# Kernel optimization log

Measured on AMD Instinct MI355X. Metric: run time of the kernel, lower is better.

The kernel has to match this reference:

```python
import jax, jax.numpy as jnp
import numpy as np

N, E, F_IN, H, C = 10000, 640000, 128, 128, 40


def setup_inputs() -> dict:
    key = jax.random.key(0)
    ks = jax.random.split(key, 8)
    x = jax.random.normal(ks[0], (N, F_IN), dtype=jnp.float32)
    edge_index = jax.random.randint(ks[1], (2, E), 0, N, dtype=jnp.int64)
    W1 = jax.random.normal(ks[2], (F_IN, H), dtype=jnp.float32) / np.sqrt(F_IN)
    b1 = jnp.zeros((H,), dtype=jnp.float32)
    W2 = jax.random.normal(ks[3], (H, H), dtype=jnp.float32) / np.sqrt(H)
    b2 = jnp.zeros((H,), dtype=jnp.float32)
    Wc = jax.random.normal(ks[4], (H, C), dtype=jnp.float32) / np.sqrt(H)
    bc = jnp.zeros((C,), dtype=jnp.float32)
    return {"x": x, "edge_index": edge_index, "W1": W1, "b1": b1,
            "W2": W2, "b2": b2, "Wc": Wc, "bc": bc}


def _gcn_conv(x, src, dst, norm, W, b):
    # GCNConv: out = D^{-1/2}(A+I)D^{-1/2} (x @ W) + b
    h = x @ W                               # [N, H]
    msg = h[src] * norm[:, None]            # gather + per-edge normalize
    out = jax.ops.segment_sum(msg, dst, num_segments=N)  # scatter-add
    return out + b


def reference(x, edge_index, W1, b1, W2, b2, Wc, bc):
    # add self-loops (as PyG GCNConv does by default)
    loops = jnp.arange(N, dtype=edge_index.dtype)
    src = jnp.concatenate([edge_index[0], loops])   # [E+N]
    dst = jnp.concatenate([edge_index[1], loops])   # [E+N]
    # symmetric normalization deg^{-1/2} with self-loops included
    deg = jax.ops.segment_sum(jnp.ones_like(dst, dtype=x.dtype), dst, num_segments=N)
    dinv = jax.lax.rsqrt(deg)                       # deg >= 1 due to self-loops
    norm = dinv[src] * dinv[dst]                    # [E+N]

    h = _gcn_conv(x, src, dst, norm, W1, b1)
    h = jax.nn.relu(h)
    h = _gcn_conv(h, src, dst, norm, W2, b2)
    logits = h @ Wc + bc                            # [N, C]
    return jax.nn.log_softmax(logits, axis=1)
```

## Files before the change

### kernel.cpp

```cpp
#include <hip/hip_runtime.h>
#include <hip/hip_fp16.h>
#include <math.h>

#define FDIM 128
#define CDIM 40
#define DMAX 192
#define NMAX 10240
#define SLICE_SHIFT 14
#define SLICE_SZ (1 << SLICE_SHIFT)

__device__ __forceinline__ uint2 pack_half4(float4 v) {
    __half2 p0 = __float22half2_rn(make_float2(v.x, v.y));
    __half2 p1 = __float22half2_rn(make_float2(v.z, v.w));
    uint2 u;
    u.x = *(unsigned int*)&p0;
    u.y = *(unsigned int*)&p1;
    return u;
}

__device__ __forceinline__ void unpack_add4(float acc[8], uint4 r) {
    __half2* p = (__half2*)&r;
    #pragma unroll
    for (int q = 0; q < 4; ++q) {
        float2 f = __half22float2(p[q]);
        acc[2 * q]     += f.x;
        acc[2 * q + 1] += f.y;
    }
}

__global__ __launch_bounds__(256) void k_hist(
        const int* __restrict__ dst, unsigned short* __restrict__ lrank,
        int* __restrict__ cnt, int e, int n) {
    __shared__ int h[NMAX];
    int tid = threadIdx.x;
    for (int i = tid; i < n; i += 256) h[i] = 0;
    __syncthreads();
    int base = (int)blockIdx.x << SLICE_SHIFT;
    int end = base + SLICE_SZ; if (end > e) end = e;
    for (int i = base + tid * 4; i < end; i += 1024) {
        if (i + 3 < end) {
            int4 d = *(const int4*)(dst + i);
            int p0 = atomicAdd(&h[d.x], 1);
            int p1 = atomicAdd(&h[d.y], 1);
            int p2 = atomicAdd(&h[d.z], 1);
            int p3 = atomicAdd(&h[d.w], 1);
            ushort4 r;
            r.x = (unsigned short)p0; r.y = (unsigned short)p1;
            r.z = (unsigned short)p2; r.w = (unsigned short)p3;
            *(ushort4*)(lrank + i) = r;
        } else {
            for (int k = i; k < end; ++k)
                lrank[k] = (unsigned short)atomicAdd(&h[dst[k]], 1);
        }
    }
    __syncthreads();
    int* c = cnt + (size_t)blockIdx.x * n;
    for (int i = tid; i < n; i += 256) c[i] = h[i];
}

__global__ __launch_bounds__(256) void k_scan(
        int* __restrict__ cnt, int* __restrict__ deg, int nslice, int n) {
    int v = blockIdx.x * 256 + threadIdx.x;
    if (v >= n) return;
    int s = 0;
    for (int b = 0; b < nslice; ++b) {
        int t = cnt[(size_t)b * n + v];
        cnt[(size_t)b * n + v] = s;
        s += t;
    }
    deg[v] = s;
}

__global__ __launch_bounds__(256) void k_mega(
        const float* __restrict__ A, const float* __restrict__ W,
        const int* __restrict__ deg, uint2* __restrict__ h16, int n,
        const int* __restrict__ src, const int* __restrict__ dst,
        const unsigned short* __restrict__ lrank, const int* __restrict__ base,
        unsigned short* __restrict__ col, int e, int gemm_blocks) {
    __shared__ float As[32][FDIM];
    int tid = threadIdx.x;
    if ((int)blockIdx.x < gemm_blocks) {
        int r0 = blockIdx.x * 32;
        for (int t = tid; t < 32 * 32; t += 256) {
            int r = t >> 5, c4 = t & 31;
            int gr = r0 + r;
            float4 v = make_float4(0.f, 0.f, 0.f, 0.f);
            if (gr < n) v = ((const float4*)A)[(size_t)gr * 32 + c4];
            ((float4*)As[r])[c4] = v;
        }
        __syncthreads();
        int cb = (tid & 31) * 4;
        int rb = (tid >> 5) * 4;
        float4 acc0 = make_float4(0,0,0,0), acc1 = acc0, acc2 = acc0, acc3 = acc0;
        for (int k = 0; k < FDIM; ++k) {
            float4 w = *(const float4*)(W + k * FDIM + cb);
            float a0 = As[rb + 0][k], a1 = As[rb + 1][k];
            float a2 = As[rb + 2][k], a3 = As[rb + 3][k];
            acc0.x += a0 * w.x; acc0.y += a0 * w.y; acc0.z += a0 * w.z; acc0.w += a0 * w.w;
            acc1.x += a1 * w.x; acc1.y += a1 * w.y; acc1.z += a1 * w.z; acc1.w += a1 * w.w;
            acc2.x += a2 * w.x; acc2.y += a2 * w.y; acc2.z += a2 * w.z; acc2.w += a2 * w.w;
            acc3.x += a3 * w.x; acc3.y += a3 * w.y; acc3.z += a3 * w.z; acc3.w += a3 * w.w;
        }
        float4 accs[4] = {acc0, acc1, acc2, acc3};
        #pragma unroll
        for (int i = 0; i < 4; ++i) {
            int gr = r0 + rb + i;
            if (gr < n) {
                float dinv = rsqrtf((float)(deg[gr] + 1));
                float4 v = accs[i];
                v.x *= dinv; v.y *= dinv; v.z *= dinv; v.w *= dinv;
                h16[(size_t)gr * 32 + (cb >> 2)] = pack_half4(v);
            }
        }
    } else {
        int g = ((int)blockIdx.x - gemm_blocks) * 256 + tid;
        int i4 = g * 4;
        if (i4 + 3 < e) {
            const int* bs = base + (size_t)(i4 >> SLICE_SHIFT) * n;
            int4 d = ((const int4*)dst)[g];
            int4 s = ((const int4*)src)[g];
            ushort4 lr = ((const ushort4*)lrank)[g];
            int p0 = bs[d.x] + lr.x;
            int p1 = bs[d.y] + lr.y;
            int p2 = bs[d.z] + lr.z;
            int p3 = bs[d.w] + lr.w;
            if (p0 < DMAX) col[(size_t)d.x * DMAX + p0] = (unsigned short)s.x;
            if (p1 < DMAX) col[(size_t)d.y * DMAX + p1] = (unsigned short)s.y;
            if (p2 < DMAX) col[(size_t)d.z * DMAX + p2] = (unsigned short)s.z;
            if (p3 < DMAX) col[(size_t)d.w * DMAX + p3] = (unsigned short)s.w;
        } else if (i4 < e) {
            for (int k = i4; k < e; ++k) {
                int d = dst[k];
                int p = base[(size_t)(k >> SLICE_SHIFT) * n + d] + lrank[k];
                if (p < DMAX) col[(size_t)d * DMAX + p] = (unsigned short)src[k];
            }
        }
    }
}

template <bool RELU>
__device__ __forceinline__ void agg_gather(
        float out8[8], const uint4* __restrict__ hs,
        const unsigned short* __restrict__ col, const int* __restrict__ deg,
        const float* __restrict__ bias, int node, int l) {
    int dn = deg[node];
    float dinv = rsqrtf((float)(dn + 1));
    if (dn > DMAX) dn = DMAX;
    const uint4* cl8 = (const uint4*)(col + (size_t)node * DMAX);
    float a0[8], a1[8];
    #pragma unroll
    for (int q = 0; q < 8; ++q) { a0[q] = 0.f; a1[q] = 0.f; }
    unpack_add4(a0, hs[(size_t)node * 16 + l]);
    int j = 0;
    for (; j + 16 <= dn; j += 16) {
        uint4 cA = cl8[(j >> 3) + 0];
        uint4 cB = cl8[(j >> 3) + 1];
        int s0 = cA.x & 0xFFFF, s1 = cA.x >> 16;
        int s2 = cA.y & 0xFFFF, s3 = cA.y >> 16;
        int s4 = cA.z & 0xFFFF, s5 = cA.z >> 16;
        int s6 = cA.w & 0xFFFF, s7 = cA.w >> 16;
        int s8 = cB.x & 0xFFFF, s9 = cB.x >> 16;
        int sa = cB.y & 0xFFFF, sb = cB.y >> 16;
        int sc = cB.z & 0xFFFF, sd = cB.z >> 16;
        int se = cB.w & 0xFFFF, sf = cB.w >> 16;
        uint4 q0 = hs[(size_t)s0 * 16 + l];
        uint4 q1 = hs[(size_t)s1 * 16 + l];
        uint4 q2 = hs[(size_t)s2 * 16 + l];
        uint4 q3 = hs[(size_t)s3 * 16 + l];
        uint4 q4 = hs[(size_t)s4 * 16 + l];
        uint4 q5 = hs[(size_t)s5 * 16 + l];
        uint4 q6 = hs[(size_t)s6 * 16 + l];
        uint4 q7 = hs[(size_t)s7 * 16 + l];
        uint4 q8 = hs[(size_t)s8 * 16 + l];
        uint4 q9 = hs[(size_t)s9 * 16 + l];
        uint4 qa = hs[(size_t)sa * 16 + l];
        uint4 qb = hs[(size_t)sb * 16 + l];
        uint4 qc = hs[(size_t)sc * 16 + l];
        uint4 qd = hs[(size_t)sd * 16 + l];
        uint4 qe = hs[(size_t)se * 16 + l];
        uint4 qf = hs[(size_t)sf * 16 + l];
        unpack_add4(a0, q0); unpack_add4(a1, q1);
        unpack_add4(a0, q2); unpack_add4(a1, q3);
        unpack_add4(a0, q4); unpack_add4(a1, q5);
        unpack_add4(a0, q6); unpack_add4(a1, q7);
        unpack_add4(a0, q8); unpack_add4(a1, q9);
        unpack_add4(a0, qa); unpack_add4(a1, qb);
        unpack_add4(a0, qc); unpack_add4(a1, qd);
        unpack_add4(a0, qe); unpack_add4(a1, qf);
    }
    for (; j + 8 <= dn; j += 8) {
        uint4 c = cl8[j >> 3];
        int s0 = c.x & 0xFFFF, s1 = c.x >> 16;
        int s2 = c.y & 0xFFFF, s3 = c.y >> 16;
        int s4 = c.z & 0xFFFF, s5 = c.z >> 16;
        int s6 = c.w & 0xFFFF, s7 = c.w >> 16;
        uint4 q0 = hs[(size_t)s0 * 16 + l];
        uint4 q1 = hs[(size_t)s1 * 16 + l];
        uint4 q2 = hs[(size_t)s2 * 16 + l];
        uint4 q3 = hs[(size_t)s3 * 16 + l];
        uint4 q4 = hs[(size_t)s4 * 16 + l];
        uint4 q5 = hs[(size_t)s5 * 16 + l];
        uint4 q6 = hs[(size_t)s6 * 16 + l];
        uint4 q7 = hs[(size_t)s7 * 16 + l];
        unpack_add4(a0, q0); unpack_add4(a1, q1);
        unpack_add4(a0, q2); unpack_add4(a1, q3);
        unpack_add4(a0, q4); unpack_add4(a1, q5);
        unpack_add4(a0, q6); unpack_add4(a1, q7);
    }
    const unsigned short* cl = col + (size_t)node * DMAX;
    for (; j < dn; ++j) unpack_add4(a0, hs[(size_t)cl[j] * 16 + l]);
    float4 b0 = ((const float4*)bias)[2 * l];
    float4 b1 = ((const float4*)bias)[2 * l + 1];
    float bb[8] = {b0.x, b0.y, b0.z, b0.w, b1.x, b1.y, b1.z, b1.w};
    #pragma unroll
    for (int q = 0; q < 8; ++q) {
        float v = dinv * (a0[q] + a1[q]) + bb[q];
        out8[q] = RELU ? fmaxf(v, 0.f) : v;
    }
}

__global__ __launch_bounds__(128) void k_agg_gemm(
        const uint4* __restrict__ hs1, const unsigned short* __restrict__ col,
        const int* __restrict__ deg, const float* __restrict__ b1,
        const float* __restrict__ W2, uint2* __restrict__ hs2, int n) {
    __shared__ float As[8][FDIM + 4];
    __shared__ float dl[8];
    int tid = threadIdx.x;
    int grp = tid >> 4, l = tid & 15;
    int node = blockIdx.x * 8 + grp;
    if (node < n) {
        float r8[8];
        agg_gather<true>(r8, hs1, col, deg, b1, node, l);
        float4* dst4 = (float4*)&As[grp][8 * l];
        dst4[0] = make_float4(r8[0], r8[1], r8[2], r8[3]);
        dst4[1] = make_float4(r8[4], r8[5], r8[6], r8[7]);
        if (l == 0) dl[grp] = rsqrtf((float)(deg[node] + 1));
    }
    __syncthreads();
    int cb = (tid & 31) * 4;
    int rb = (tid >> 5) * 2;
    float4 acc0 = make_float4(0,0,0,0), acc1 = acc0;
    for (int k = 0; k < FDIM; ++k) {
        float4 w = *(const float4*)(W2 + k * FDIM + cb);
        float x0 = As[rb][k], x1 = As[rb + 1][k];
        acc0.x += x0 * w.x; acc0.y += x0 * w.y; acc0.z += x0 * w.z; acc0.w += x0 * w.w;
        acc1.x += x1 * w.x; acc1.y += x1 * w.y; acc1.z += x1 * w.z; acc1.w += x1 * w.w;
    }
    int g0 = blockIdx.x * 8 + rb;
    if (g0 < n) {
        float s = dl[rb];
        float4 v = acc0;
        v.x *= s; v.y *= s; v.z *= s; v.w *= s;
        hs2[(size_t)g0 * 32 + (cb >> 2)] = pack_half4(v);
    }
    if (g0 + 1 < n) {
        float s = dl[rb + 1];
        float4 v = acc1;
        v.x *= s; v.y *= s; v.z *= s; v.w *= s;
        hs2[(size_t)(g0 + 1) * 32 + (cb >> 2)] = pack_half4(v);
    }
}

__global__ __launch_bounds__(128) void k_agg_cls(
        const uint4* __restrict__ hs2, const unsigned short* __restrict__ col,
        const int* __restrict__ deg, const float* __restrict__ b2,
        const float* __restrict__ Wc, const float* __restrict__ bc,
        float* __restrict__ out, int n) {
    __shared__ float As[8][FDIM + 4];
    int tid = threadIdx.x;
    int grp = tid >> 4, l = tid & 15;
    int node = blockIdx.x * 8 + grp;
    if (node < n) {
        float r8[8];
        agg_gather<false>(r8, hs2, col, deg, b2, node, l);
        float4* dst4 = (float4*)&As[grp][8 * l];
        dst4[0] = make_float4(r8[0], r8[1], r8[2], r8[3]);
        dst4[1] = make_float4(r8[4], r8[5], r8[6], r8[7]);
    }
    __syncthreads();
    int wv = tid >> 6, lane = tid & 63;
    #pragma unroll
    for (int ii = 0; ii < 4; ++ii) {
        int li = wv * 4 + ii;
        int nd = blockIdx.x * 8 + li;
        if (nd >= n) continue;
        const float* row = As[li];
        int c = (lane < CDIM) ? lane : (lane - 24);
        float acc = bc[c];
        for (int k = 0; k < FDIM; k += 4) {
            float a0 = row[k + 0], a1 = row[k + 1];
            float a2 = row[k + 2], a3 = row[k + 3];
            acc += a0 * Wc[(k + 0) * CDIM + c];
            acc += a1 * Wc[(k + 1) * CDIM + c];
            acc += a2 * Wc[(k + 2) * CDIM + c];
            acc += a3 * Wc[(k + 3) * CDIM + c];
        }
        float lv = (lane < CDIM) ? acc : -INFINITY;
        float m = lv;
        for (int off = 32; off > 0; off >>= 1) m = fmaxf(m, __shfl_down(m, off));
        m = __shfl(m, 0);
        float e = (lane < CDIM) ? expf(lv - m) : 0.0f;
        float s = e;
        for (int off = 32; off > 0; off >>= 1) s += __shfl_down(s, off);
        s = __shfl(s, 0);
        if (lane < CDIM) out[(size_t)nd * CDIM + lane] = lv - m - logf(s);
    }
}


extern "C" void kernel_launch(void* const* d_in, const int* in_sizes, int n_in,
                              void* d_out, int out_size, void* d_ws, size_t ws_size,
                              hipStream_t stream) {
    const float* x  = (const float*)d_in[0];
    const int*   ei = (const int*)d_in[1];
    const float* W1 = (const float*)d_in[2];
    const float* b1 = (const float*)d_in[3];
    const float* W2 = (const float*)d_in[4];
    const float* b2 = (const float*)d_in[5];
    const float* Wc = (const float*)d_in[6];
    const float* bc = (const float*)d_in[7];
    float* out = (float*)d_out;

    const int N = in_sizes[0] / FDIM;
    const int E = in_sizes[1] / 2;
    const int* srcp = ei;
    const int* dstp = ei + E;
    const int NSLICE = (E + SLICE_SZ - 1) >> SLICE_SHIFT;

    char* ws = (char*)d_ws;
    auto alloc = [&](size_t bytes) {
        char* p = ws;
        ws += (bytes + 255) & ~(size_t)255;
        return p;
    };
    int*            deg   = (int*)           alloc((size_t)N * 4);
    int*            cnt   = (int*)           alloc((size_t)NSLICE * N * 4);
    unsigned short* lrank = (unsigned short*)alloc((size_t)E * 2);
    unsigned short* col   = (unsigned short*)alloc((size_t)N * DMAX * 2);
    uint4*          h1h   = (uint4*)         alloc((size_t)N * 256);
    uint4*          h2h   = (uint4*)         alloc((size_t)N * 256);

    k_hist<<<NSLICE, 256, 0, stream>>>(dstp, lrank, cnt, E, N);

    k_scan<<<(N + 255) / 256, 256, 0, stream>>>(cnt, deg, NSLICE, N);

    int gb = (N + 31) / 32;
    int fb = (E / 4 + 255) / 256;
    k_mega<<<gb + fb, 256, 0, stream>>>(
        x, W1, deg, (uint2*)h1h, N, srcp, dstp, lrank, cnt, col, E, gb);

    k_agg_gemm<<<(N + 7) / 8, 128, 0, stream>>>(
        h1h, col, deg, b1, W2, (uint2*)h2h, N);

    k_agg_cls<<<(N + 7) / 8, 128, 0, stream>>>(
        h2h, col, deg, b2, Wc, bc, out, N);
}
```

Baseline: 159.5 us.

## Overlap layer-1 GEMM with histogram, shrink slices, use fma_mix accumulation

Moves the first x@W1 GEMM into the histogram kernel as extra blocks that write fp32 results, so it no longer waits on the degree scan. The later fill kernel gains blocks that scale by dinv and pack the result to fp16. Slices shrink from 16K to 4K edges to give the histogram more parallel blocks. The aggregation loop now prefetches column indices one step ahead and accumulates fp16 with inline v_fma_mix_f32 instead of converting then adding. The costs are an extra fp32 N×128 round trip through memory and a scan over four times as many slices.

```diff
diff --git a/kernel.cpp b/kernel.cpp
--- a/kernel.cpp
+++ b/kernel.cpp
@@ -6,7 +6,7 @@
 #define CDIM 40
 #define DMAX 192
 #define NMAX 10240
-#define SLICE_SHIFT 14
+#define SLICE_SHIFT 12
 #define SLICE_SZ (1 << SLICE_SHIFT)
 
 __device__ __forceinline__ uint2 pack_half4(float4 v) {
@@ -18,69 +18,54 @@
     return u;
 }
 
-__device__ __forceinline__ void unpack_add4(float acc[8], uint4 r) {
-    __half2* p = (__half2*)&r;
-    #pragma unroll
-    for (int q = 0; q < 4; ++q) {
-        float2 f = __half22float2(p[q]);
-        acc[2 * q]     += f.x;
-        acc[2 * q + 1] += f.y;
-    }
+__device__ __forceinline__ void fmix_add4(float a[8], uint4 r) {
+    asm("v_fma_mix_f32 %0, %8, 1.0, %0 op_sel:[0,0,0] op_sel_hi:[1,0,0]\n\t"
+        "v_fma_mix_f32 %1, %8, 1.0, %1 op_sel:[1,0,0] op_sel_hi:[1,0,0]\n\t"
+        "v_fma_mix_f32 %2, %9, 1.0, %2 op_sel:[0,0,0] op_sel_hi:[1,0,0]\n\t"
+        "v_fma_mix_f32 %3, %9, 1.0, %3 op_sel:[1,0,0] op_sel_hi:[1,0,0]\n\t"
+        "v_fma_mix_f32 %4, %10, 1.0, %4 op_sel:[0,0,0] op_sel_hi:[1,0,0]\n\t"
+        "v_fma_mix_f32 %5, %10, 1.0, %5 op_sel:[1,0,0] op_sel_hi:[1,0,0]\n\t"
+        "v_fma_mix_f32 %6, %11, 1.0, %6 op_sel:[0,0,0] op_sel_hi:[1,0,0]\n\t"
+        "v_fma_mix_f32 %7, %11, 1.0, %7 op_sel:[1,0,0] op_sel_hi:[1,0,0]"
+        : "+v"(a[0]), "+v"(a[1]), "+v"(a[2]), "+v"(a[3]),
+          "+v"(a[4]), "+v"(a[5]), "+v"(a[6]), "+v"(a[7])
+        : "v"(r.x), "v"(r.y), "v"(r.z), "v"(r.w));
 }
 
 __global__ __launch_bounds__(256) void k_hist(
         const int* __restrict__ dst, unsigned short* __restrict__ lrank,
-        int* __restrict__ cnt, int e, int n) {
+        int* __restrict__ cnt, int e, int n, int nslice,
+        const float* __restrict__ A, const float* __restrict__ W,
+        float* __restrict__ h1f) {
     __shared__ int h[NMAX];
     int tid = threadIdx.x;
-    for (int i = tid; i < n; i += 256) h[i] = 0;
-    __syncthreads();
-    int base = (int)blockIdx.x << SLICE_SHIFT;
-    int end = base + SLICE_SZ; if (end > e) end = e;
-    for (int i = base + tid * 4; i < end; i += 1024) {
-        if (i + 3 < end) {
-            int4 d = *(const int4*)(dst + i);
-            int p0 = atomicAdd(&h[d.x], 1);
-            int p1 = atomicAdd(&h[d.y], 1);
-            int p2 = atomicAdd(&h[d.z], 1);
-            int p3 = atomicAdd(&h[d.w], 1);
-            ushort4 r;
-            r.x = (unsigned short)p0; r.y = (unsigned short)p1;
-            r.z = (unsigned short)p2; r.w = (unsigned short)p3;
-            *(ushort4*)(lrank + i) = r;
-        } else {
-            for (int k = i; k < end; ++k)
-                lrank[k] = (unsigned short)atomicAdd(&h[dst[k]], 1);
-        }
-    }
-    __syncthreads();
-    int* c = cnt + (size_t)blockIdx.x * n;
-    for (int i = tid; i < n; i += 256) c[i] = h[i];
-}
-
-__global__ __launch_bounds__(256) void k_scan(
-        int* __restrict__ cnt, int* __restrict__ deg, int nslice, int n) {
-    int v = blockIdx.x * 256 + threadIdx.x;
-    if (v >= n) return;
-    int s = 0;
-    for (int b = 0; b < nslice; ++b) {
-        int t = cnt[(size_t)b * n + v];
-        cnt[(size_t)b * n + v] = s;
-        s += t;
-    }
-    deg[v] = s;
-}
-
-__global__ __launch_bounds__(256) void k_mega(
-        const float* __restrict__ A, const float* __restrict__ W,
-        const int* __restrict__ deg, uint2* __restrict__ h16, int n,
-        const int* __restrict__ src, const int* __restrict__ dst,
-        const unsigned short* __restrict__ lrank, const int* __restrict__ base,
-        unsigned short* __restrict__ col, int e, int gemm_blocks) {
-    __shared__ float As[32][FDIM];
-    int tid = threadIdx.x;
-    if ((int)blockIdx.x < gemm_blocks) {
-        int r0 = blockIdx.x * 32;
+    if ((int)blockIdx.x < nslice) {
+        for (int i = tid; i < n; i += 256) h[i] = 0;
+        __syncthreads();
+        int base = (int)blockIdx.x << SLICE_SHIFT;
+        int end = base + SLICE_SZ; if (end > e) end = e;
+        for (int i = base + tid * 4; i < end; i += 1024) {
+            if (i + 3 < end) {
+                int4 d = *(const int4*)(dst + i);
+                int p0 = atomicAdd(&h[d.x], 1);
+                int p1 = atomicAdd(&h[d.y], 1);
+                int p2 = atomicAdd(&h[d.z], 1);
+                int p3 = atomicAdd(&h[d.w], 1);
+                ushort4 r;
+                r.x = (unsigned short)p0; r.y = (unsigned short)p1;
+                r.z = (unsigned short)p2; r.w = (unsigned short)p3;
+                *(ushort4*)(lrank + i) = r;
+            } else {
+                for (int k = i; k < end; ++k)
+                    lrank[k] = (unsigned short)atomicAdd(&h[dst[k]], 1);
+            }
+        }
+        __syncthreads();
+        int* c = cnt + (size_t)blockIdx.x * n;
+        for (int i = tid; i < n; i += 256) c[i] = h[i];
+    } else {
+        float (*As)[FDIM] = (float (*)[FDIM])h;
+        int r0 = ((int)blockIdx.x - nslice) * 32;
         for (int t = tid; t < 32 * 32; t += 256) {
             int r = t >> 5, c4 = t & 31;
             int gr = r0 + r;
@@ -105,15 +90,33 @@
         #pragma unroll
         for (int i = 0; i < 4; ++i) {
             int gr = r0 + rb + i;
-            if (gr < n) {
-                float dinv = rsqrtf((float)(deg[gr] + 1));
-                float4 v = accs[i];
-                v.x *= dinv; v.y *= dinv; v.z *= dinv; v.w *= dinv;
-                h16[(size_t)gr * 32 + (cb >> 2)] = pack_half4(v);
-            }
-        }
-    } else {
-        int g = ((int)blockIdx.x - gemm_blocks) * 256 + tid;
+            if (gr < n) ((float4*)h1f)[(size_t)gr * 32 + (cb >> 2)] = accs[i];
+        }
+    }
+}
+
+__global__ __launch_bounds__(256) void k_scan(
+        int* __restrict__ cnt, int* __restrict__ deg, int nslice, int n) {
+    int v = blockIdx.x * 256 + threadIdx.x;
+    if (v >= n) return;
+    int s = 0;
+    for (int b = 0; b < nslice; ++b) {
+        int t = cnt[(size_t)b * n + v];
+        cnt[(size_t)b * n + v] = s;
+        s += t;
+    }
+    deg[v] = s;
+}
+
+__global__ __launch_bounds__(256) void k_mega(
+        const int* __restrict__ src, const int* __restrict__ dst,
+        const unsigned short* __restrict__ lrank, const int* __restrict__ base,
+        unsigned short* __restrict__ col, int e,
+        const float* __restrict__ h1f, const int* __restrict__ deg,
+        uint2* __restrict__ h16, int n, int fill_blocks) {
+    int tid = threadIdx.x;
+    if ((int)blockIdx.x < fill_blocks) {
+        int g = (int)blockIdx.x * 256 + tid;
         int i4 = g * 4;
         if (i4 + 3 < e) {
             const int* bs = base + (size_t)(i4 >> SLICE_SHIFT) * n;
@@ -130,10 +133,21 @@
             if (p3 < DMAX) col[(size_t)d.w * DMAX + p3] = (unsigned short)s.w;
         } else if (i4 < e) {
             for (int k = i4; k < e; ++k) {
-                int d = dst[k];
-                int p = base[(size_t)(k >> SLICE_SHIFT) * n + d] + lrank[k];
-                if (p < DMAX) col[(size_t)d * DMAX + p] = (unsigned short)src[k];
+                int dd = dst[k];
+                int p = base[(size_t)(k >> SLICE_SHIFT) * n + dd] + lrank[k];
+                if (p < DMAX) col[(size_t)dd * DMAX + p] = (unsigned short)src[k];
             }
+        }
+    } else {
+        int g = ((int)blockIdx.x - fill_blocks) * 256 + tid;
+        int t4 = n * 32;
+        int stride = ((int)gridDim.x - fill_blocks) * 256;
+        for (int idx = g; idx < t4; idx += stride) {
+            int node = idx >> 5;
+            float dinv = rsqrtf((float)(deg[node] + 1));
+            float4 v = ((const float4*)h1f)[idx];
+            v.x *= dinv; v.y *= dinv; v.z *= dinv; v.w *= dinv;
+            h16[idx] = pack_half4(v);
         }
     }
 }
@@ -150,43 +164,48 @@
     float a0[8], a1[8];
     #pragma unroll
     for (int q = 0; q < 8; ++q) { a0[q] = 0.f; a1[q] = 0.f; }
-    unpack_add4(a0, hs[(size_t)node * 16 + l]);
+    fmix_add4(a0, hs[(size_t)node * 16 + l]);
     int j = 0;
-    for (; j + 16 <= dn; j += 16) {
-        uint4 cA = cl8[(j >> 3) + 0];
-        uint4 cB = cl8[(j >> 3) + 1];
-        int s0 = cA.x & 0xFFFF, s1 = cA.x >> 16;
-        int s2 = cA.y & 0xFFFF, s3 = cA.y >> 16;
-        int s4 = cA.z & 0xFFFF, s5 = cA.z >> 16;
-        int s6 = cA.w & 0xFFFF, s7 = cA.w >> 16;
-        int s8 = cB.x & 0xFFFF, s9 = cB.x >> 16;
-        int sa = cB.y & 0xFFFF, sb = cB.y >> 16;
-        int sc = cB.z & 0xFFFF, sd = cB.z >> 16;
-        int se = cB.w & 0xFFFF, sf = cB.w >> 16;
-        uint4 q0 = hs[(size_t)s0 * 16 + l];
-        uint4 q1 = hs[(size_t)s1 * 16 + l];
-        uint4 q2 = hs[(size_t)s2 * 16 + l];
-        uint4 q3 = hs[(size_t)s3 * 16 + l];
-        uint4 q4 = hs[(size_t)s4 * 16 + l];
-        uint4 q5 = hs[(size_t)s5 * 16 + l];
-        uint4 q6 = hs[(size_t)s6 * 16 + l];
-        uint4 q7 = hs[(size_t)s7 * 16 + l];
-        uint4 q8 = hs[(size_t)s8 * 16 + l];
-        uint4 q9 = hs[(size_t)s9 * 16 + l];
-        uint4 qa = hs[(size_t)sa * 16 + l];
-        uint4 qb = hs[(size_t)sb * 16 + l];
-        uint4 qc = hs[(size_t)sc * 16 + l];
-        uint4 qd = hs[(size_t)sd * 16 + l];
-        uint4 qe = hs[(size_t)se * 16 + l];
-        uint4 qf = hs[(size_t)sf * 16 + l];
-        unpack_add4(a0, q0); unpack_add4(a1, q1);
-        unpack_add4(a0, q2); unpack_add4(a1, q3);
-        unpack_add4(a0, q4); unpack_add4(a1, q5);
-        unpack_add4(a0, q6); unpack_add4(a1, q7);
-        unpack_add4(a0, q8); unpack_add4(a1, q9);
-        unpack_add4(a0, qa); unpack_add4(a1, qb);
-        unpack_add4(a0, qc); unpack_add4(a1, qd);
-        unpack_add4(a0, qe); unpack_add4(a1, qf);
+    if (j + 16 <= dn) {
+        uint4 cA = cl8[0];
+        uint4 cB = cl8[1];
+        for (; j + 16 <= dn; j += 16) {
+            uint4 nA = cl8[(j >> 3) + 2];
+            uint4 nB = cl8[(j >> 3) + 3];
+            int s0 = cA.x & 0xFFFF, s1 = cA.x >> 16;
+            int s2 = cA.y & 0xFFFF, s3 = cA.y >> 16;
+            int s4 = cA.z & 0xFFFF, s5 = cA.z >> 16;
+            int s6 = cA.w & 0xFFFF, s7 = cA.w >> 16;
+            int s8 = cB.x & 0xFFFF, s9 = cB.x >> 16;
+            int sa = cB.y & 0xFFFF, sb = cB.y >> 16;
+            int sc = cB.z & 0xFFFF, sd = cB.z >> 16;
+            int se = cB.w & 0xFFFF, sf = cB.w >> 16;
+            uint4 q0 = hs[(size_t)s0 * 16 + l];
+            uint4 q1 = hs[(size_t)s1 * 16 + l];
+            uint4 q2 = hs[(size_t)s2 * 16 + l];
+            uint4 q3 = hs[(size_t)s3 * 16 + l];
+            uint4 q4 = hs[(size_t)s4 * 16 + l];
+            uint4 q5 = hs[(size_t)s5 * 16 + l];
+            uint4 q6 = hs[(size_t)s6 * 16 + l];
+            uint4 q7 = hs[(size_t)s7 * 16 + l];
+            uint4 q8 = hs[(size_t)s8 * 16 + l];
+            uint4 q9 = hs[(size_t)s9 * 16 + l];
+            uint4 qa = hs[(size_t)sa * 16 + l];
+            uint4 qb = hs[(size_t)sb * 16 + l];
+            uint4 qc = hs[(size_t)sc * 16 + l];
+            uint4 qd = hs[(size_t)sd * 16 + l];
+            uint4 qe = hs[(size_t)se * 16 + l];
+            uint4 qf = hs[(size_t)sf * 16 + l];
+            fmix_add4(a0, q0); fmix_add4(a1, q1);
+            fmix_add4(a0, q2); fmix_add4(a1, q3);
+            fmix_add4(a0, q4); fmix_add4(a1, q5);
+            fmix_add4(a0, q6); fmix_add4(a1, q7);
+            fmix_add4(a0, q8); fmix_add4(a1, q9);
+            fmix_add4(a0, qa); fmix_add4(a1, qb);
+            fmix_add4(a0, qc); fmix_add4(a1, qd);
+            fmix_add4(a0, qe); fmix_add4(a1, qf);
+            cA = nA; cB = nB;
+        }
     }
     for (; j + 8 <= dn; j += 8) {
         uint4 c = cl8[j >> 3];
@@ -202,16 +221,16 @@
         uint4 q5 = hs[(size_t)s5 * 16 + l];
         uint4 q6 = hs[(size_t)s6 * 16 + l];
         uint4 q7 = hs[(size_t)s7 * 16 + l];
-        unpack_add4(a0, q0); unpack_add4(a1, q1);
-        unpack_add4(a0, q2); unpack_add4(a1, q3);
-        unpack_add4(a0, q4); unpack_add4(a1, q5);
-        unpack_add4(a0, q6); unpack_add4(a1, q7);
+        fmix_add4(a0, q0); fmix_add4(a1, q1);
+        fmix_add4(a0, q2); fmix_add4(a1, q3);
+        fmix_add4(a0, q4); fmix_add4(a1, q5);
+        fmix_add4(a0, q6); fmix_add4(a1, q7);
     }
     const unsigned short* cl = col + (size_t)node * DMAX;
-    for (; j < dn; ++j) unpack_add4(a0, hs[(size_t)cl[j] * 16 + l]);
+    for (; j < dn; ++j) fmix_add4(a0, hs[(size_t)cl[j] * 16 + l]);
     float4 b0 = ((const float4*)bias)[2 * l];
-    float4 b1 = ((const float4*)bias)[2 * l + 1];
-    float bb[8] = {b0.x, b0.y, b0.z, b0.w, b1.x, b1.y, b1.z, b1.w};
+    float4 b1v = ((const float4*)bias)[2 * l + 1];
+    float bb[8] = {b0.x, b0.y, b0.z, b0.w, b1v.x, b1v.y, b1v.z, b1v.w};
     #pragma unroll
     for (int q = 0; q < 8; ++q) {
         float v = dinv * (a0[q] + a1[q]) + bb[q];
@@ -337,17 +356,20 @@
     int*            cnt   = (int*)           alloc((size_t)NSLICE * N * 4);
     unsigned short* lrank = (unsigned short*)alloc((size_t)E * 2);
     unsigned short* col   = (unsigned short*)alloc((size_t)N * DMAX * 2);
+    float*          h1f   = (float*)         alloc((size_t)N * FDIM * 4);
     uint4*          h1h   = (uint4*)         alloc((size_t)N * 256);
     uint4*          h2h   = (uint4*)         alloc((size_t)N * 256);
 
-    k_hist<<<NSLICE, 256, 0, stream>>>(dstp, lrank, cnt, E, N);
+    int gb = (N + 31) / 32;
+    k_hist<<<NSLICE + gb, 256, 0, stream>>>(dstp, lrank, cnt, E, N, NSLICE,
+                                            x, W1, h1f);
 
     k_scan<<<(N + 255) / 256, 256, 0, stream>>>(cnt, deg, NSLICE, N);
 
-    int gb = (N + 31) / 32;
     int fb = (E / 4 + 255) / 256;
-    k_mega<<<gb + fb, 256, 0, stream>>>(
-        x, W1, deg, (uint2*)h1h, N, srcp, dstp, lrank, cnt, col, E, gb);
+    int sb = (N * 32 + 4 * 256 - 1) / (4 * 256);
+    k_mega<<<fb + sb, 256, 0, stream>>>(
+        srcp, dstp, lrank, cnt, col, E, h1f, deg, (uint2*)h1h, N, fb);
 
     k_agg_gemm<<<(N + 7) / 8, 128, 0, stream>>>(
         h1h, col, deg, b1, W2, (uint2*)h2h, N);
```

New measurement: 183.9 us. +15.3%, slower.

## Split each node's neighbor gather across two half-warps with shuffle reduction

Applied to the files above, without the earlier changes.

Each node is now aggregated by 32 lanes instead of 16: two 16-lane halves take alternating 8-neighbor chunks of the column list and combine their partial sums with a shuffle-xor. Blocks cover 4 nodes instead of 8, so the grid doubles and the dense W2 and classifier stages each handle fewer rows per block. The goal is more memory-level parallelism and a shorter serial gather chain per node. The cost is fewer nodes per block, which means more redundant W2 and Wc loads overall plus the extra shuffle.

```diff
diff --git a/kernel.cpp b/kernel.cpp
--- a/kernel.cpp
+++ b/kernel.cpp
@@ -142,7 +142,7 @@
 __device__ __forceinline__ void agg_gather(
         float out8[8], const uint4* __restrict__ hs,
         const unsigned short* __restrict__ col, const int* __restrict__ deg,
-        const float* __restrict__ bias, int node, int l) {
+        const float* __restrict__ bias, int node, int l, int g) {
     int dn = deg[node];
     float dinv = rsqrtf((float)(dn + 1));
     if (dn > DMAX) dn = DMAX;
@@ -150,11 +150,12 @@
     float a0[8], a1[8];
     #pragma unroll
     for (int q = 0; q < 8; ++q) { a0[q] = 0.f; a1[q] = 0.f; }
-    unpack_add4(a0, hs[(size_t)node * 16 + l]);
-    int j = 0;
-    for (; j + 16 <= dn; j += 16) {
-        uint4 cA = cl8[(j >> 3) + 0];
-        uint4 cB = cl8[(j >> 3) + 1];
+    if (g) unpack_add4(a0, hs[(size_t)node * 16 + l]);
+    int nch = dn >> 3;
+    int t = g;
+    for (; t + 2 < nch; t += 4) {
+        uint4 cA = cl8[t];
+        uint4 cB = cl8[t + 2];
         int s0 = cA.x & 0xFFFF, s1 = cA.x >> 16;
         int s2 = cA.y & 0xFFFF, s3 = cA.y >> 16;
         int s4 = cA.z & 0xFFFF, s5 = cA.z >> 16;
@@ -188,8 +189,8 @@
         unpack_add4(a0, qc); unpack_add4(a1, qd);
         unpack_add4(a0, qe); unpack_add4(a1, qf);
     }
-    for (; j + 8 <= dn; j += 8) {
-        uint4 c = cl8[j >> 3];
+    if (t < nch) {
+        uint4 c = cl8[t];
         int s0 = c.x & 0xFFFF, s1 = c.x >> 16;
         int s2 = c.y & 0xFFFF, s3 = c.y >> 16;
         int s4 = c.z & 0xFFFF, s5 = c.z >> 16;
@@ -207,14 +208,19 @@
         unpack_add4(a0, q4); unpack_add4(a1, q5);
         unpack_add4(a0, q6); unpack_add4(a1, q7);
     }
-    const unsigned short* cl = col + (size_t)node * DMAX;
-    for (; j < dn; ++j) unpack_add4(a0, hs[(size_t)cl[j] * 16 + l]);
+    if (g == 0) {
+        const unsigned short* cl = col + (size_t)node * DMAX;
+        for (int j = nch * 8; j < dn; ++j)
+            unpack_add4(a0, hs[(size_t)cl[j] * 16 + l]);
+    }
     float4 b0 = ((const float4*)bias)[2 * l];
-    float4 b1 = ((const float4*)bias)[2 * l + 1];
-    float bb[8] = {b0.x, b0.y, b0.z, b0.w, b1.x, b1.y, b1.z, b1.w};
+    float4 b1v = ((const float4*)bias)[2 * l + 1];
+    float bb[8] = {b0.x, b0.y, b0.z, b0.w, b1v.x, b1v.y, b1v.z, b1v.w};
     #pragma unroll
     for (int q = 0; q < 8; ++q) {
-        float v = dinv * (a0[q] + a1[q]) + bb[q];
+        float v = a0[q] + a1[q];
+        v += __shfl_xor(v, 16);
+        v = dinv * v + bb[q];
         out8[q] = RELU ? fmaxf(v, 0.f) : v;
     }
 }
@@ -223,41 +229,37 @@
         const uint4* __restrict__ hs1, const unsigned short* __restrict__ col,
         const int* __restrict__ deg, const float* __restrict__ b1,
         const float* __restrict__ W2, uint2* __restrict__ hs2, int n) {
-    __shared__ float As[8][FDIM + 4];
-    __shared__ float dl[8];
+    __shared__ float As[4][FDIM + 4];
+    __shared__ float dl[4];
     int tid = threadIdx.x;
-    int grp = tid >> 4, l = tid & 15;
-    int node = blockIdx.x * 8 + grp;
+    int grp = tid >> 5, l32 = tid & 31;
+    int l = l32 & 15, g = l32 >> 4;
+    int node = blockIdx.x * 4 + grp;
     if (node < n) {
         float r8[8];
-        agg_gather<true>(r8, hs1, col, deg, b1, node, l);
-        float4* dst4 = (float4*)&As[grp][8 * l];
-        dst4[0] = make_float4(r8[0], r8[1], r8[2], r8[3]);
-        dst4[1] = make_float4(r8[4], r8[5], r8[6], r8[7]);
-        if (l == 0) dl[grp] = rsqrtf((float)(deg[node] + 1));
+        agg_gather<true>(r8, hs1, col, deg, b1, node, l, g);
+        if (g == 0) {
+            float4* dst4 = (float4*)&As[grp][8 * l];
+            dst4[0] = make_float4(r8[0], r8[1], r8[2], r8[3]);
+            dst4[1] = make_float4(r8[4], r8[5], r8[6], r8[7]);
+        }
+        if (l32 == 0) dl[grp] = rsqrtf((float)(deg[node] + 1));
     }
     __syncthreads();
     int cb = (tid & 31) * 4;
-    int rb = (tid >> 5) * 2;
-    float4 acc0 = make_float4(0,0,0,0), acc1 = acc0;
+    int rb = tid >> 5;
+    float4 acc = make_float4(0, 0, 0, 0);
     for (int k = 0; k < FDIM; ++k) {
         float4 w = *(const float4*)(W2 + k * FDIM + cb);
-        float x0 = As[rb][k], x1 = As[rb + 1][k];
-        acc0.x += x0 * w.x; acc0.y += x0 * w.y; acc0.z += x0 * w.z; acc0.w += x0 * w.w;
-        acc1.x += x1 * w.x; acc1.y += x1 * w.y; acc1.z += x1 * w.z; acc1.w += x1 * w.w;
-    }
-    int g0 = blockIdx.x * 8 + rb;
+        float x0 = As[rb][k];
+        acc.x += x0 * w.x; acc.y += x0 * w.y; acc.z += x0 * w.z; acc.w += x0 * w.w;
+    }
+    int g0 = blockIdx.x * 4 + rb;
     if (g0 < n) {
         float s = dl[rb];
-        float4 v = acc0;
+        float4 v = acc;
         v.x *= s; v.y *= s; v.z *= s; v.w *= s;
         hs2[(size_t)g0 * 32 + (cb >> 2)] = pack_half4(v);
-    }
-    if (g0 + 1 < n) {
-        float s = dl[rb + 1];
-        float4 v = acc1;
-        v.x *= s; v.y *= s; v.z *= s; v.w *= s;
-        hs2[(size_t)(g0 + 1) * 32 + (cb >> 2)] = pack_half4(v);
     }
 }
 
@@ -266,23 +268,26 @@
         const int* __restrict__ deg, const float* __restrict__ b2,
         const float* __restrict__ Wc, const float* __restrict__ bc,
         float* __restrict__ out, int n) {
-    __shared__ float As[8][FDIM + 4];
+    __shared__ float As[4][FDIM + 4];
     int tid = threadIdx.x;
-    int grp = tid >> 4, l = tid & 15;
-    int node = blockIdx.x * 8 + grp;
+    int grp = tid >> 5, l32 = tid & 31;
+    int l = l32 & 15, g = l32 >> 4;
+    int node = blockIdx.x * 4 + grp;
     if (node < n) {
         float r8[8];
-        agg_gather<false>(r8, hs2, col, deg, b2, node, l);
-        float4* dst4 = (float4*)&As[grp][8 * l];
-        dst4[0] = make_float4(r8[0], r8[1], r8[2], r8[3]);
-        dst4[1] = make_float4(r8[4], r8[5], r8[6], r8[7]);
+        agg_gather<false>(r8, hs2, col, deg, b2, node, l, g);
+        if (g == 0) {
+            float4* dst4 = (float4*)&As[grp][8 * l];
+            dst4[0] = make_float4(r8[0], r8[1], r8[2], r8[3]);
+            dst4[1] = make_float4(r8[4], r8[5], r8[6], r8[7]);
+        }
     }
     __syncthreads();
     int wv = tid >> 6, lane = tid & 63;
     #pragma unroll
-    for (int ii = 0; ii < 4; ++ii) {
-        int li = wv * 4 + ii;
-        int nd = blockIdx.x * 8 + li;
+    for (int ii = 0; ii < 2; ++ii) {
+        int li = wv * 2 + ii;
+        int nd = blockIdx.x * 4 + li;
         if (nd >= n) continue;
         const float* row = As[li];
         int c = (lane < CDIM) ? lane : (lane - 24);
@@ -349,9 +354,9 @@
     k_mega<<<gb + fb, 256, 0, stream>>>(
         x, W1, deg, (uint2*)h1h, N, srcp, dstp, lrank, cnt, col, E, gb);
 
-    k_agg_gemm<<<(N + 7) / 8, 128, 0, stream>>>(
+    k_agg_gemm<<<(N + 3) / 4, 128, 0, stream>>>(
         h1h, col, deg, b1, W2, (uint2*)h2h, N);
 
-    k_agg_cls<<<(N + 7) / 8, 128, 0, stream>>>(
+    k_agg_cls<<<(N + 3) / 4, 128, 0, stream>>>(
         h2h, col, deg, b2, Wc, bc, out, N);
 }
```

Measured after the change: 170.5 us. +6.9%, slower.
